# Performance work log

Measured on AMD Instinct MI355X. Metric: run time of the kernel, lower is better.

The kernel has to match this reference:

```python
import jax, jax.numpy as jnp
import numpy as np

DIM = 3456      # visual_dim
E = 1024        # embed_dim = dim_head*heads = 128*8
H = 8
D = E // H
LN_EPS = 1e-5


def _mlp(x, w1, b1, w2, b2):
    # nn.Sequential(Linear, GELU(exact), Linear)
    h = jax.nn.gelu(x @ w1.T + b1, approximate=False)
    return h @ w2.T + b2


def _ln(x, g, b):
    m = jnp.mean(x, axis=-1, keepdims=True)
    v = jnp.mean((x - m) ** 2, axis=-1, keepdims=True)
    return (x - m) * jax.lax.rsqrt(v + LN_EPS) * g + b


def setup_inputs() -> dict:
    key = jax.random.key(0)
    ks = jax.random.split(key, 24)
    std = 0.02
    d = {"x": jax.random.normal(ks[0], (5, 729, DIM), dtype=jnp.float32)}
    i = 1
    for name in ("q", "k", "v"):
        d[f"{name}_w1"] = std * jax.random.normal(ks[i], (E, DIM), dtype=jnp.float32); i += 1
        d[f"{name}_b1"] = jnp.zeros((E,), jnp.float32)
        d[f"{name}_w2"] = std * jax.random.normal(ks[i], (E, E), dtype=jnp.float32); i += 1
        d[f"{name}_b2"] = jnp.zeros((E,), jnp.float32)
        d[f"ln_{name}_g"] = jnp.ones((E,), jnp.float32)
        d[f"ln_{name}_b"] = jnp.zeros((E,), jnp.float32)
    d["in_proj_w"] = std * jax.random.normal(ks[i], (3 * E, E), dtype=jnp.float32); i += 1
    d["in_proj_b"] = jnp.zeros((3 * E,), jnp.float32)
    d["out_proj_w"] = std * jax.random.normal(ks[i], (E, E), dtype=jnp.float32); i += 1
    d["out_proj_b"] = jnp.zeros((E,), jnp.float32)
    d["to_out_w"] = std * jax.random.normal(ks[i], (DIM, E), dtype=jnp.float32)
    return d


def reference(x,
              q_w1, q_b1, q_w2, q_b2, ln_q_g, ln_q_b,
              k_w1, k_b1, k_w2, k_b2, ln_k_g, ln_k_b,
              v_w1, v_b1, v_w2, v_b2, ln_v_g, ln_v_b,
              in_proj_w, in_proj_b, out_proj_w, out_proj_b, to_out_w):
    t, hw, c = x.shape
    # spatial_temporal pattern: x_multi = x, no interpolation.
    # q/k/v: MLP -> LN -> permute(1,0,2) -> divide_feature -> flatten.
    # divide_feature is a pure permutation of tokens; all tokens end up in a
    # single (L, 1, E) attention, so full attention over the flattened
    # (hw, t) token order computes the identical result.
    q = _ln(_mlp(x, q_w1, q_b1, q_w2, q_b2), ln_q_g, ln_q_b)  # (t, hw, E)
    k = _ln(_mlp(x, k_w1, k_b1, k_w2, k_b2), ln_k_g, ln_k_b)
    v = _ln(_mlp(x, v_w1, v_b1, v_w2, v_b2), ln_v_g, ln_v_b)
    L = t * hw
    q = q.transpose(1, 0, 2).reshape(L, E)  # (hw*t, E), (h,w,t)-major order
    k = k.transpose(1, 0, 2).reshape(L, E)
    v = v.transpose(1, 0, 2).reshape(L, E)
    # nn.MultiheadAttention with packed in_proj
    qp = (q @ in_proj_w[:E].T + in_proj_b[:E]).reshape(L, H, D)
    kp = (k @ in_proj_w[E:2 * E].T + in_proj_b[E:2 * E]).reshape(L, H, D)
    vp = (v @ in_proj_w[2 * E:].T + in_proj_b[2 * E:]).reshape(L, H, D)
    scale = 1.0 / jnp.sqrt(jnp.asarray(D, q.dtype))
    scores = jnp.einsum('qhd,khd->hqk', qp, kp) * scale  # (H, L, L)
    attn = jax.nn.softmax(scores, axis=-1)
    o = jnp.einsum('hqk,khd->qhd', attn, vp).reshape(L, E)
    o = o @ out_proj_w.T + out_proj_b
    o = o.reshape(hw, t, E).transpose(1, 0, 2)  # (t, hw, E)
    out = o @ to_out_w.T                         # (t, hw, c)
    return x + out
```

## Files before the change

kernel.cpp:

```cpp
#include <hip/hip_runtime.h>
#include <hip/hip_bf16.h>

#define L_TOK 3645
#define MP    3712
#define DIMV  3456
#define EDIM  1024

typedef __attribute__((ext_vector_type(8))) short bf8;
typedef __attribute__((ext_vector_type(4))) short s4v;
typedef __attribute__((ext_vector_type(4))) float f4;

__device__ __forceinline__ short f2b(float f) {
  union { float f; unsigned u; } v; v.f = f;
  unsigned r = v.u + 0x7fffu + ((v.u >> 16) & 1u);
  return (short)(r >> 16);
}
__device__ __forceinline__ float b2f(short s) {
  union { unsigned u; float f; } v; v.u = ((unsigned)(unsigned short)s) << 16;
  return v.f;
}
__device__ __forceinline__ void gld16(const void* g, void* l) {
  __builtin_amdgcn_global_load_lds(
      (const __attribute__((address_space(1))) void*)(unsigned long long)g,
      (__attribute__((address_space(3))) void*)(unsigned)(unsigned long long)l,
      16, 0, 0);
}

__global__ __launch_bounds__(256) void k_cvt(const float* __restrict__ src,
                                             short* __restrict__ dst, int n4) {
  int i = blockIdx.x * 256 + threadIdx.x;
  if (i >= n4) return;
  float4 v = ((const float4*)src)[i];
  s4v o; o[0] = f2b(v.x); o[1] = f2b(v.y); o[2] = f2b(v.z); o[3] = f2b(v.w);
  ((s4v*)dst)[i] = o;
}
__global__ __launch_bounds__(256) void k_cvt_pad(const float* __restrict__ src,
                                                 short* __restrict__ dst, int n4src, int n4tot) {
  int i = blockIdx.x * 256 + threadIdx.x;
  if (i >= n4tot) return;
  s4v o; o[0] = 0; o[1] = 0; o[2] = 0; o[3] = 0;
  if (i < n4src) {
    float4 v = ((const float4*)src)[i];
    o[0] = f2b(v.x); o[1] = f2b(v.y); o[2] = f2b(v.z); o[3] = f2b(v.w);
  }
  ((s4v*)dst)[i] = o;
}

#define GM_GELU   0
#define GM_BIAS   1
#define GM_QSCALE 2
#define GM_RESID  3

template<int MODE>
__global__ __launch_bounds__(512, 2)
void k_gemm2(const short* __restrict__ A, long sA,
             const short* __restrict__ B, long sB,
             const float* __restrict__ bias0, const float* __restrict__ bias1,
             const float* __restrict__ bias2,
             void* __restrict__ Cout, long sC,
             int N, int K, const float* __restrict__ resid)
{
  __shared__ short L[2][2][2][8192];
  const int tid = threadIdx.x;
  const int z = blockIdx.z;
  const int brow = blockIdx.y * 256;
  const int bcol = blockIdx.x * 256;
  const short* Ab = A + (long)z * sA;
  const short* Bb = B + (long)z * sB;
  const float* bias = (z == 0) ? bias0 : (z == 1 ? bias1 : bias2);

  const int wave = tid >> 6, lane = tid & 63;
  const int lg = lane >> 4, lc = lane & 15;
  const int wm = wave >> 2, wn = wave & 3;

  const int r0 = tid >> 3, x0 = tid & 7;
  const int c1 = tid + 512;
  const int r1 = c1 >> 3, x1 = c1 & 7;
  const short* pa[2][2];
  const short* pb[2][2];
#pragma unroll
  for (int half = 0; half < 2; ++half) {
    int ra0 = brow + half * 128 + r0; if (ra0 > MP - 1) ra0 = MP - 1;
    int ra1 = brow + half * 128 + r1; if (ra1 > MP - 1) ra1 = MP - 1;
    int rb0 = bcol + half * 128 + r0; if (rb0 > N - 1) rb0 = N - 1;
    int rb1 = bcol + half * 128 + r1; if (rb1 > N - 1) rb1 = N - 1;
    pa[half][0] = Ab + (long)ra0 * K + ((x0 ^ (r0 & 7)) * 8);
    pa[half][1] = Ab + (long)ra1 * K + ((x1 ^ (r1 & 7)) * 8);
    pb[half][0] = Bb + (long)rb0 * K + ((x0 ^ (r0 & 7)) * 8);
    pb[half][1] = Bb + (long)rb1 * K + ((x1 ^ (r1 & 7)) * 8);
  }

  f4 acc[8][4];
  f4 zero = {0.f, 0.f, 0.f, 0.f};
#pragma unroll
  for (int i = 0; i < 8; ++i)
#pragma unroll
    for (int j = 0; j < 4; ++j) acc[i][j] = zero;

  auto STG = [&](int bufi, int ab, int half) {
    if (ab == 0) {
      gld16(pa[half][0], &L[bufi][0][half][tid * 8]);
      gld16(pa[half][1], &L[bufi][0][half][c1 * 8]);
      pa[half][0] += 64; pa[half][1] += 64;
    } else {
      gld16(pb[half][0], &L[bufi][1][half][tid * 8]);
      gld16(pb[half][1], &L[bufi][1][half][c1 * 8]);
      pb[half][0] += 64; pb[half][1] += 64;
    }
  };

  const int NT = K >> 6;
  STG(0, 0, 0); STG(0, 0, 1); STG(0, 1, 0); STG(0, 1, 1);

  const int bhalf = wn >> 1, brw = (wn & 1) * 64;
  bf8 bfr[4][2];

  for (int kt = 0; kt < NT; ++kt) {
    const int buf = kt & 1, nb = buf ^ 1;
    const bool more = (kt + 1 < NT);
#pragma unroll
    for (int p = 0; p < 4; ++p) {
      if (p == 0) {
        if (more) { STG(nb, 0, 0); asm volatile("s_waitcnt vmcnt(2)" ::: "memory"); }
        else      { asm volatile("s_waitcnt vmcnt(0)" ::: "memory"); }
        __builtin_amdgcn_sched_barrier(0);
        __builtin_amdgcn_s_barrier();
        __builtin_amdgcn_sched_barrier(0);
#pragma unroll
        for (int nf = 0; nf < 4; ++nf)
#pragma unroll
          for (int ks = 0; ks < 2; ++ks) {
            int row = brw + nf * 16 + lc;
            int seg = (ks * 4 + lg) ^ (row & 7);
            bfr[nf][ks] = *(const bf8*)&L[buf][1][bhalf][row * 64 + seg * 8];
          }
      } else {
        if (more) STG(nb, p >> 1, p & 1);
      }
      bf8 af[2][2];
#pragma unroll
      for (int m2 = 0; m2 < 2; ++m2)
#pragma unroll
        for (int ks = 0; ks < 2; ++ks) {
          int row = p * 32 + m2 * 16 + lc;
          int seg = (ks * 4 + lg) ^ (row & 7);
          af[m2][ks] = *(const bf8*)&L[buf][0][wm][row * 64 + seg * 8];
        }
      asm volatile("s_waitcnt lgkmcnt(0)" ::: "memory");
      __builtin_amdgcn_sched_barrier(0);
      __builtin_amdgcn_s_setprio(1);
#pragma unroll
      for (int m2 = 0; m2 < 2; ++m2)
#pragma unroll
        for (int nf = 0; nf < 4; ++nf)
#pragma unroll
          for (int ks = 0; ks < 2; ++ks)
            acc[p * 2 + m2][nf] = __builtin_amdgcn_mfma_f32_16x16x32_bf16(
                af[m2][ks], bfr[nf][ks], acc[p * 2 + m2][nf], 0, 0, 0);
      __builtin_amdgcn_s_setprio(0);
      __builtin_amdgcn_sched_barrier(0);
      __builtin_amdgcn_s_barrier();
    }
  }

  if (MODE == GM_RESID) {
    float* C = (float*)Cout;
#pragma unroll
    for (int nf = 0; nf < 4; ++nf) {
      int col = bcol + wn * 64 + nf * 16 + lc;
#pragma unroll
      for (int mf = 0; mf < 8; ++mf)
#pragma unroll
        for (int r = 0; r < 4; ++r) {
          int row = brow + wm * 128 + mf * 16 + lg * 4 + r;
          if (row < L_TOK && col < N)
            C[(long)row * N + col] = acc[mf][nf][r] + resid[(long)row * N + col];
        }
    }
  } else {
    short* C = (short*)Cout + (long)z * sC;
    const float alpha = (MODE == GM_QSCALE && z == 0) ? 0.08838834764831845f : 1.0f;
#pragma unroll
    for (int nf = 0; nf < 4; ++nf) {
      int col = bcol + wn * 64 + nf * 16 + lc;
      float bv = bias[col];
#pragma unroll
      for (int mf = 0; mf < 8; ++mf)
#pragma unroll
        for (int r = 0; r < 4; ++r) {
          int row = brow + wm * 128 + mf * 16 + lg * 4 + r;
          float v = acc[mf][nf][r] + bv;
          if (MODE == GM_GELU) v = 0.5f * v * (1.f + erff(v * 0.70710678118654752f));
          v *= alpha;
          if (row < MP) C[(long)row * EDIM + col] = f2b(v);
        }
    }
  }
}

template<int MODE>
__global__ __launch_bounds__(256)
void k_gemm(const short* __restrict__ A, long sA,
            const short* __restrict__ B, long sB,
            const float* __restrict__ bias0, const float* __restrict__ bias1,
            const float* __restrict__ bias2,
            void* __restrict__ Cout, long sC,
            int N, int K, const float* __restrict__ resid)
{
  __shared__ short As[2][128 * 32];
  __shared__ short Bs[2][128 * 32];
  const int tid  = threadIdx.x;
  const int z    = blockIdx.z;
  const int nwg  = gridDim.x * gridDim.y;
  const int orig = blockIdx.y * gridDim.x + blockIdx.x;
  const int qq   = nwg >> 3, rr = nwg & 7;
  const int xcd  = orig & 7, ofs = orig >> 3;
  const int swz  = (xcd < rr ? xcd * (qq + 1) : rr * (qq + 1) + (xcd - rr) * qq) + ofs;
  const int brow = (swz / gridDim.x) * 128;
  const int bcol = (swz % gridDim.x) * 128;

  const short* Ab = A + (long)z * sA;
  const short* Bb = B + (long)z * sB;
  const float* bias = (z == 0) ? bias0 : (z == 1 ? bias1 : bias2);

  const int wave = tid >> 6, lane = tid & 63;
  const int lg = lane >> 4, lc = lane & 15;
  const int m0 = (wave >> 1) * 64, n0 = (wave & 1) * 64;

  const int r0 = tid >> 2, seg = tid & 3;
  const int r1 = r0 + 64;
  const int so0 = (seg ^ ((r0 >> 1) & 3)) * 8;
  const int so1 = (seg ^ ((r1 >> 1) & 3)) * 8;
  const short* pA0 = Ab + (long)(brow + r0) * K + so0;
  const short* pA1 = Ab + (long)(brow + r1) * K + so1;
  const short* pB0 = Bb + (long)(bcol + r0) * K + so0;
  const short* pB1 = Bb + (long)(bcol + r1) * K + so1;

  f4 acc[4][4];
  f4 zero = {0.f, 0.f, 0.f, 0.f};
#pragma unroll
  for (int i = 0; i < 4; ++i)
#pragma unroll
    for (int j = 0; j < 4; ++j) acc[i][j] = zero;

  auto STAGE = [&](int buf) {
    gld16(pA0, &As[buf][tid * 8]);
    gld16(pA1, &As[buf][(tid + 256) * 8]);
    gld16(pB0, &Bs[buf][tid * 8]);
    gld16(pB1, &Bs[buf][(tid + 256) * 8]);
    pA0 += 32; pA1 += 32; pB0 += 32; pB1 += 32;
  };

  const int NT = K >> 5;
  STAGE(0);
  for (int t = 0; t < NT; ++t) {
    const int buf = t & 1;
    asm volatile("s_waitcnt vmcnt(0)" ::: "memory");
    __builtin_amdgcn_sched_barrier(0);
    __builtin_amdgcn_s_barrier();
    if (t + 1 < NT) STAGE((t + 1) & 1);
    const short* Al = &As[buf][0];
    const short* Bl = &Bs[buf][0];
    bf8 af[4], bfr[4];
#pragma unroll
    for (int mi = 0; mi < 4; ++mi) {
      int r = m0 + mi * 16 + lc;
      af[mi] = *(const bf8*)&Al[r * 32 + ((lg ^ ((r >> 1) & 3)) * 8)];
    }
#pragma unroll
    for (int ni = 0; ni < 4; ++ni) {
      int r = n0 + ni * 16 + lc;
      bfr[ni] = *(const bf8*)&Bl[r * 32 + ((lg ^ ((r >> 1) & 3)) * 8)];
    }
    __builtin_amdgcn_s_setprio(1);
#pragma unroll
    for (int mi = 0; mi < 4; ++mi)
#pragma unroll
      for (int ni = 0; ni < 4; ++ni)
        acc[mi][ni] = __builtin_amdgcn_mfma_f32_16x16x32_bf16(af[mi], bfr[ni], acc[mi][ni], 0, 0, 0);
    __builtin_amdgcn_s_setprio(0);
    __builtin_amdgcn_sched_barrier(0);
  }

  if (MODE == GM_RESID) {
    float* C = (float*)Cout;
#pragma unroll
    for (int ni = 0; ni < 4; ++ni) {
      int col = bcol + n0 + ni * 16 + lc;
#pragma unroll
      for (int mi = 0; mi < 4; ++mi)
#pragma unroll
        for (int r = 0; r < 4; ++r) {
          int row = brow + m0 + mi * 16 + lg * 4 + r;
          if (row < L_TOK)
            C[(long)row * N + col] = acc[mi][ni][r] + resid[(long)row * N + col];
        }
    }
  } else {
    short* C = (short*)Cout + (long)z * sC;
    const float alpha = (MODE == GM_QSCALE && z == 0) ? 0.08838834764831845f : 1.0f;
#pragma unroll
    for (int ni = 0; ni < 4; ++ni) {
      int col = bcol + n0 + ni * 16 + lc;
      float bv = bias[col];
#pragma unroll
      for (int mi = 0; mi < 4; ++mi)
#pragma unroll
        for (int r = 0; r < 4; ++r) {
          int row = brow + m0 + mi * 16 + lg * 4 + r;
          float v = acc[mi][ni][r] + bv;
          if (MODE == GM_GELU) v = 0.5f * v * (1.f + erff(v * 0.70710678118654752f));
          v *= alpha;
          C[(long)row * EDIM + col] = f2b(v);
        }
    }
  }
}

__global__ __launch_bounds__(256)
void k_ln(const short* __restrict__ A, short* __restrict__ Y,
          const float* __restrict__ g0, const float* __restrict__ g1, const float* __restrict__ g2,
          const float* __restrict__ b0, const float* __restrict__ b1, const float* __restrict__ b2)
{
  const int row = blockIdx.x, z = blockIdx.y;
  const float* g = (z == 0) ? g0 : (z == 1 ? g1 : g2);
  const float* b = (z == 0) ? b0 : (z == 1 ? b1 : b2);
  const short* a = A + ((long)z * MP + row) * EDIM;
  short* y = Y + ((long)z * MP + row) * EDIM;
  const int t = threadIdx.x;
  s4v v = *(const s4v*)&a[t * 4];
  float x0 = b2f(v[0]), x1 = b2f(v[1]), x2 = b2f(v[2]), x3 = b2f(v[3]);
  float s = x0 + x1 + x2 + x3;
  float q = x0 * x0 + x1 * x1 + x2 * x2 + x3 * x3;
#pragma unroll
  for (int off = 1; off < 64; off <<= 1) { s += __shfl_xor(s, off); q += __shfl_xor(q, off); }
  __shared__ float rs[4], rq[4];
  if ((t & 63) == 0) { rs[t >> 6] = s; rq[t >> 6] = q; }
  __syncthreads();
  s = rs[0] + rs[1] + rs[2] + rs[3];
  q = rq[0] + rq[1] + rq[2] + rq[3];
  float mean = s * (1.f / 1024.f);
  float var  = q * (1.f / 1024.f) - mean * mean;
  float rstd = rsqrtf(var + 1e-5f);
  s4v o;
#pragma unroll
  for (int j = 0; j < 4; ++j) {
    int col = t * 4 + j;
    o[j] = f2b((b2f(v[j]) - mean) * rstd * g[col] + b[col]);
  }
  *(s4v*)&y[t * 4] = o;
}

__global__ __launch_bounds__(256)
void k_vtrans(const short* __restrict__ vp, short* __restrict__ vpT)
{
  const int kb = blockIdx.x * 64, h = blockIdx.y;
  __shared__ short T[64 * 128];
  const int tid = threadIdx.x;
#pragma unroll
  for (int i = 0; i < 4; ++i) {
    int c = tid + 256 * i;
    int r = c >> 4, x = c & 15;
    bf8 val = *(const bf8*)&vp[(long)(kb + r) * EDIM + h * 128 + x * 8];
    *(bf8*)&T[r * 128 + ((x ^ (r & 7)) * 8)] = val;
  }
  __syncthreads();
#pragma unroll
  for (int i = 0; i < 4; ++i) {
    int c = tid + 256 * i;
    int dr = c >> 3, x = c & 7;
    short tmp[8];
#pragma unroll
    for (int e = 0; e < 8; ++e) {
      int kv = x * 8 + e;
      tmp[e] = T[kv * 128 + (((dr >> 3) ^ (kv & 7)) << 3) + (dr & 7)];
    }
    *(bf8*)&vpT[((long)h * 128 + dr) * MP + kb + x * 8] = *(bf8*)tmp;
  }
}

__global__ __launch_bounds__(256)
void k_attn(const short* __restrict__ qp, const short* __restrict__ kp,
            const short* __restrict__ vpT,
            short* __restrict__ op0, short* __restrict__ op1,
            float* __restrict__ lsums)
{
  const int bx = blockIdx.x;
  const int h = bx & 7;
  const int t2 = bx >> 3;
  const int qi = t2 % 29, sp = t2 / 29;
  const int qb = qi * 128;
  short* opart = sp ? op1 : op0;
  const int t0 = sp ? 29 : 0, t1 = sp ? 57 : 29;

  const int tid = threadIdx.x, wave = tid >> 6, lane = tid & 63;
  const int lg = lane >> 4, lc = lane & 15;
  __shared__ short Ks[2][64 * 128];
  __shared__ short Vs[2][128 * 64];
  __shared__ short Ps[4][32 * 64];

  const int q0 = qb + wave * 32;
  bf8 qf[2][4];
#pragma unroll
  for (int g = 0; g < 2; ++g)
#pragma unroll
    for (int d4 = 0; d4 < 4; ++d4)
      qf[g][d4] = *(const bf8*)&qp[(long)(q0 + g * 16 + lc) * EDIM + h * 128 + d4 * 32 + lg * 8];

  f4 oacc[2][8];
  f4 zero = {0.f, 0.f, 0.f, 0.f};
#pragma unroll
  for (int g = 0; g < 2; ++g)
#pragma unroll
    for (int dt = 0; dt < 8; ++dt) oacc[g][dt] = zero;
  float lsum0 = 0.f, lsum1 = 0.f;

  auto STAGE = [&](short* ksb, short* vsb, int kb) {
#pragma unroll
    for (int i = 0; i < 4; ++i) {
      int c = tid + 256 * i; int r = c >> 4, x = c & 15;
      gld16(&kp[(long)(kb + r) * EDIM + h * 128 + (x ^ (r & 7)) * 8], &ksb[c * 8]);
    }
#pragma unroll
    for (int i = 0; i < 4; ++i) {
      int c = tid + 256 * i; int dr = c >> 3, x = c & 7;
      gld16(&vpT[((long)h * 128 + dr) * MP + kb + (x ^ (dr & 7)) * 8], &vsb[c * 8]);
    }
  };

  STAGE(Ks[t0 & 1], Vs[t0 & 1], t0 * 64);

  for (int t = t0; t < t1; ++t) {
    const int kb = t * 64;
    const short* ksb = Ks[t & 1];
    const short* vsb = Vs[t & 1];
    __builtin_amdgcn_s_barrier();
    if (t + 1 < t1) {
      STAGE(Ks[(t + 1) & 1], Vs[(t + 1) & 1], kb + 64);
      asm volatile("s_waitcnt vmcnt(8)" ::: "memory");
    } else {
      asm volatile("s_waitcnt vmcnt(0)" ::: "memory");
    }
    __builtin_amdgcn_sched_barrier(0);
    __builtin_amdgcn_s_barrier();
    __builtin_amdgcn_sched_barrier(0);

#pragma unroll
    for (int s = 0; s < 4; ++s) {
      const int krow = s * 16 + lc;
      bf8 kf[4];
#pragma unroll
      for (int d4 = 0; d4 < 4; ++d4)
        kf[d4] = *(const bf8*)&ksb[krow * 128 + (((d4 * 4 + lg) ^ (krow & 7)) * 8)];
      f4 sa0 = zero, sa1 = zero;
      __builtin_amdgcn_s_setprio(1);
#pragma unroll
      for (int d4 = 0; d4 < 4; ++d4) {
        sa0 = __builtin_amdgcn_mfma_f32_16x16x32_bf16(kf[d4], qf[0][d4], sa0, 0, 0, 0);
        sa1 = __builtin_amdgcn_mfma_f32_16x16x32_bf16(kf[d4], qf[1][d4], sa1, 0, 0, 0);
      }
      __builtin_amdgcn_s_setprio(0);
      const int kvb = kb + s * 16 + lg * 4;
#pragma unroll
      for (int g = 0; g < 2; ++g) {
        f4 sa = g ? sa1 : sa0;
        float p[4];
#pragma unroll
        for (int r = 0; r < 4; ++r) {
          float e = __expf(sa[r]);
          p[r] = (kvb + r < L_TOK) ? e : 0.f;
          if (g) lsum1 += p[r]; else lsum0 += p[r];
        }
        s4v pk; pk[0] = f2b(p[0]); pk[1] = f2b(p[1]); pk[2] = f2b(p[2]); pk[3] = f2b(p[3]);
        *(s4v*)&Ps[wave][(g * 16 + lc) * 64 + ((s * 16 + lg * 4) ^ ((lc & 7) << 3))] = pk;
      }
    }
    bf8 pf[2][2];
#pragma unroll
    for (int g = 0; g < 2; ++g) {
      pf[g][0] = *(const bf8*)&Ps[wave][(g * 16 + lc) * 64 + ((lg * 8) ^ ((lc & 7) << 3))];
      pf[g][1] = *(const bf8*)&Ps[wave][(g * 16 + lc) * 64 + ((32 + lg * 8) ^ ((lc & 7) << 3))];
    }
#pragma unroll
    for (int dt = 0; dt < 8; ++dt) {
      const int vrow = dt * 16 + lc;
      bf8 vf0 = *(const bf8*)&vsb[vrow * 64 + ((lg ^ (vrow & 7)) * 8)];
      bf8 vf1 = *(const bf8*)&vsb[vrow * 64 + (((4 + lg) ^ (vrow & 7)) * 8)];
      __builtin_amdgcn_s_setprio(1);
      oacc[0][dt] = __builtin_amdgcn_mfma_f32_16x16x32_bf16(pf[0][0], vf0, oacc[0][dt], 0, 0, 0);
      oacc[0][dt] = __builtin_amdgcn_mfma_f32_16x16x32_bf16(pf[0][1], vf1, oacc[0][dt], 0, 0, 0);
      oacc[1][dt] = __builtin_amdgcn_mfma_f32_16x16x32_bf16(pf[1][0], vf0, oacc[1][dt], 0, 0, 0);
      oacc[1][dt] = __builtin_amdgcn_mfma_f32_16x16x32_bf16(pf[1][1], vf1, oacc[1][dt], 0, 0, 0);
      __builtin_amdgcn_s_setprio(0);
    }
    __builtin_amdgcn_sched_barrier(0);
  }

  lsum0 += __shfl_xor(lsum0, 16);
  lsum0 += __shfl_xor(lsum0, 32);
  lsum1 += __shfl_xor(lsum1, 16);
  lsum1 += __shfl_xor(lsum1, 32);
  if (lg == 0) {
    lsums[((sp * 8) + h) * MP + q0 + lc]      = lsum0;
    lsums[((sp * 8) + h) * MP + q0 + 16 + lc] = lsum1;
  }
#pragma unroll
  for (int g = 0; g < 2; ++g)
#pragma unroll
    for (int dt = 0; dt < 8; ++dt)
#pragma unroll
      for (int r = 0; r < 4; ++r) {
        int orow = q0 + g * 16 + lg * 4 + r;
        opart[(long)orow * EDIM + h * 128 + dt * 16 + lc] = f2b(oacc[g][dt][r]);
      }
}

__global__ __launch_bounds__(256)
void k_comb(const short* __restrict__ p0, const short* __restrict__ p1,
            const float* __restrict__ ls, short* __restrict__ ob)
{
  int i = blockIdx.x * 256 + threadIdx.x;
  int q = i >> 7;
  int h = (i & 127) >> 4;
  float rinv = 1.f / (ls[h * MP + q] + ls[(8 + h) * MP + q]);
  bf8 a = ((const bf8*)p0)[i];
  bf8 b = ((const bf8*)p1)[i];
  bf8 o;
#pragma unroll
  for (int j = 0; j < 8; ++j) o[j] = f2b((b2f(a[j]) + b2f(b[j])) * rinv);
  ((bf8*)ob)[i] = o;
}

extern "C" void kernel_launch(void* const* d_in, const int* in_sizes, int n_in,
                              void* d_out, int out_size, void* d_ws, size_t ws_size,
                              hipStream_t stream)
{
  const float* x   = (const float*)d_in[0];
  const float* ipb = (const float*)d_in[20];
  const float* opb = (const float*)d_in[22];

  char* ws = (char*)d_ws;
  short* regA = (short*)(ws + 0);
  short* regB = (short*)(ws + 25657344);
  short* w1b  = (short*)(ws + 48463872);
  short* w2b  = (short*)(ws + 69697536);
  short* wpb  = (short*)(ws + 75988992);
  short* wob  = (short*)(ws + 82280448);
  short* wtb  = (short*)(ws + 84377600);
  short* vpT  = (short*)(ws + 91455488);

  short* xb  = regA;
  short* h1  = regB;
  short* aln = regA;
  short* lnq = regB;
  short* proj = regA;
  short* ob  = regB;
  short* o2  = (short*)(ws + 33259520);
  short* pt1 = o2;
  short* pt0 = (short*)(ws + 40861696);
  float* lsums = (float*)(ws + 22806528);

  k_cvt_pad<<<12528, 256, 0, stream>>>(x, xb, 3149280, 3207168);
  k_cvt<<<3456, 256, 0, stream>>>((const float*)d_in[1],  w1b,            884736);
  k_cvt<<<3456, 256, 0, stream>>>((const float*)d_in[7],  w1b + 3538944,  884736);
  k_cvt<<<3456, 256, 0, stream>>>((const float*)d_in[13], w1b + 7077888,  884736);
  k_cvt<<<1024, 256, 0, stream>>>((const float*)d_in[3],  w2b,            262144);
  k_cvt<<<1024, 256, 0, stream>>>((const float*)d_in[9],  w2b + 1048576,  262144);
  k_cvt<<<1024, 256, 0, stream>>>((const float*)d_in[15], w2b + 2097152,  262144);
  k_cvt<<<3072, 256, 0, stream>>>((const float*)d_in[19], wpb,            786432);
  k_cvt<<<1024, 256, 0, stream>>>((const float*)d_in[21], wob,            262144);
  k_cvt<<<3456, 256, 0, stream>>>((const float*)d_in[23], wtb,            884736);

  dim3 gg3(4, 15, 3);
  k_gemm2<GM_GELU><<<gg3, 512, 0, stream>>>(xb, 0, w1b, 3538944,
      (const float*)d_in[2], (const float*)d_in[8], (const float*)d_in[14],
      h1, (long)MP * EDIM, EDIM, DIMV, nullptr);
  k_gemm2<GM_BIAS><<<gg3, 512, 0, stream>>>(h1, (long)MP * EDIM, w2b, 1048576,
      (const float*)d_in[4], (const float*)d_in[10], (const float*)d_in[16],
      aln, (long)MP * EDIM, EDIM, EDIM, nullptr);
  dim3 gl(MP, 3);
  k_ln<<<gl, 256, 0, stream>>>(aln, lnq,
      (const float*)d_in[5], (const float*)d_in[11], (const float*)d_in[17],
      (const float*)d_in[6], (const float*)d_in[12], (const float*)d_in[18]);
  k_gemm2<GM_QSCALE><<<gg3, 512, 0, stream>>>(lnq, (long)MP * EDIM, wpb, 1048576,
      ipb, ipb + 1024, ipb + 2048,
      proj, (long)MP * EDIM, EDIM, EDIM, nullptr);
  dim3 gt(MP / 64, 8);
  k_vtrans<<<gt, 256, 0, stream>>>(proj + 2L * MP * EDIM, vpT);
  k_attn<<<29 * 2 * 8, 256, 0, stream>>>(proj, proj + (long)MP * EDIM, vpT,
      pt0, pt1, lsums);
  k_comb<<<(MP * EDIM / 8) / 256, 256, 0, stream>>>(pt0, pt1, lsums, ob);
  dim3 g1(8, 29, 1);
  k_gemm<GM_BIAS><<<g1, 256, 0, stream>>>(ob, 0, wob, 0,
      opb, opb, opb, o2, 0, EDIM, EDIM, nullptr);
  dim3 gg5(14, 15, 1);
  k_gemm2<GM_RESID><<<gg5, 512, 0, stream>>>(o2, 0, wtb, 0,
      nullptr, nullptr, nullptr, d_out, 0, DIMV, EDIM, x);
}
```

Before: 452.1 us.

## Replace 256x256 GEMM kernel with 128x256 tiles and XCD-aware block swizzle

Replaces the 512-thread 256x256-tile GEMM with a 256-thread 128x256-tile kernel that uses a K-step of 32, a simpler double-buffered loop and an XCD-aware workgroup remap. It is used for the first MLP layer and the final to_out projection. The second MLP layer and the in-projection fall back to the existing 128-tile k_gemm. The aim is more workgroups to fill the CUs and better L2 locality per XCD. The cost is less data reuse per tile and a coarser pipeline with a full vmcnt(0) wait every iteration.

New measurement: 526.5 us. 1.16x slower.

```diff
diff --git a/kernel.cpp b/kernel.cpp
--- a/kernel.cpp
+++ b/kernel.cpp
@@ -52,42 +52,43 @@
 #define GM_RESID  3
 
 template<int MODE>
-__global__ __launch_bounds__(512, 2)
-void k_gemm2(const short* __restrict__ A, long sA,
+__global__ __launch_bounds__(256)
+void k_gemm3(const short* __restrict__ A, long sA,
              const short* __restrict__ B, long sB,
              const float* __restrict__ bias0, const float* __restrict__ bias1,
              const float* __restrict__ bias2,
              void* __restrict__ Cout, long sC,
              int N, int K, const float* __restrict__ resid)
 {
-  __shared__ short L[2][2][2][8192];
-  const int tid = threadIdx.x;
-  const int z = blockIdx.z;
-  const int brow = blockIdx.y * 256;
-  const int bcol = blockIdx.x * 256;
+  __shared__ short As[2][128 * 32];
+  __shared__ short Bs[2][256 * 32];
+  const int tid  = threadIdx.x;
+  const int z    = blockIdx.z;
+  const int nwg  = gridDim.x * gridDim.y;
+  const int orig = blockIdx.y * gridDim.x + blockIdx.x;
+  const int qq   = nwg >> 3, rr = nwg & 7;
+  const int xcd  = orig & 7, ofs = orig >> 3;
+  const int swz  = (xcd < rr ? xcd * (qq + 1) : rr * (qq + 1) + (xcd - rr) * qq) + ofs;
+  const int brow = (swz / gridDim.x) * 128;
+  const int bcol = (swz % gridDim.x) * 256;
+
   const short* Ab = A + (long)z * sA;
   const short* Bb = B + (long)z * sB;
   const float* bias = (z == 0) ? bias0 : (z == 1 ? bias1 : bias2);
 
   const int wave = tid >> 6, lane = tid & 63;
   const int lg = lane >> 4, lc = lane & 15;
-  const int wm = wave >> 2, wn = wave & 3;
-
-  const int r0 = tid >> 3, x0 = tid & 7;
-  const int c1 = tid + 512;
-  const int r1 = c1 >> 3, x1 = c1 & 7;
-  const short* pa[2][2];
-  const short* pb[2][2];
-#pragma unroll
-  for (int half = 0; half < 2; ++half) {
-    int ra0 = brow + half * 128 + r0; if (ra0 > MP - 1) ra0 = MP - 1;
-    int ra1 = brow + half * 128 + r1; if (ra1 > MP - 1) ra1 = MP - 1;
-    int rb0 = bcol + half * 128 + r0; if (rb0 > N - 1) rb0 = N - 1;
-    int rb1 = bcol + half * 128 + r1; if (rb1 > N - 1) rb1 = N - 1;
-    pa[half][0] = Ab + (long)ra0 * K + ((x0 ^ (r0 & 7)) * 8);
-    pa[half][1] = Ab + (long)ra1 * K + ((x1 ^ (r1 & 7)) * 8);
-    pb[half][0] = Bb + (long)rb0 * K + ((x0 ^ (r0 & 7)) * 8);
-    pb[half][1] = Bb + (long)rb1 * K + ((x1 ^ (r1 & 7)) * 8);
+
+  const int rA0 = tid >> 2, seg = tid & 3;
+  const int rA1 = rA0 + 64;
+  const short* pA0 = Ab + (long)(brow + rA0) * K + ((seg ^ ((rA0 >> 1) & 3)) * 8);
+  const short* pA1 = Ab + (long)(brow + rA1) * K + ((seg ^ ((rA1 >> 1) & 3)) * 8);
+  const short* pB[4];
+#pragma unroll
+  for (int j = 0; j < 4; ++j) {
+    int rB = (tid >> 2) + j * 64;
+    int rb = bcol + rB; if (rb > N - 1) rb = N - 1;
+    pB[j] = Bb + (long)rb * K + ((seg ^ ((rB >> 1) & 3)) * 8);
   }
 
   f4 acc[8][4];
@@ -97,82 +98,56 @@
 #pragma unroll
     for (int j = 0; j < 4; ++j) acc[i][j] = zero;
 
-  auto STG = [&](int bufi, int ab, int half) {
-    if (ab == 0) {
-      gld16(pa[half][0], &L[bufi][0][half][tid * 8]);
-      gld16(pa[half][1], &L[bufi][0][half][c1 * 8]);
-      pa[half][0] += 64; pa[half][1] += 64;
-    } else {
-      gld16(pb[half][0], &L[bufi][1][half][tid * 8]);
-      gld16(pb[half][1], &L[bufi][1][half][c1 * 8]);
-      pb[half][0] += 64; pb[half][1] += 64;
+  auto STAGE = [&](int buf) {
+    gld16(pA0, &As[buf][tid * 8]);         pA0 += 32;
+    gld16(pA1, &As[buf][(tid + 256) * 8]); pA1 += 32;
+#pragma unroll
+    for (int j = 0; j < 4; ++j) {
+      gld16(pB[j], &Bs[buf][(tid + j * 256) * 8]);
+      pB[j] += 32;
     }
   };
 
-  const int NT = K >> 6;
-  STG(0, 0, 0); STG(0, 0, 1); STG(0, 1, 0); STG(0, 1, 1);
-
-  const int bhalf = wn >> 1, brw = (wn & 1) * 64;
-  bf8 bfr[4][2];
-
-  for (int kt = 0; kt < NT; ++kt) {
-    const int buf = kt & 1, nb = buf ^ 1;
-    const bool more = (kt + 1 < NT);
-#pragma unroll
-    for (int p = 0; p < 4; ++p) {
-      if (p == 0) {
-        if (more) { STG(nb, 0, 0); asm volatile("s_waitcnt vmcnt(2)" ::: "memory"); }
-        else      { asm volatile("s_waitcnt vmcnt(0)" ::: "memory"); }
-        __builtin_amdgcn_sched_barrier(0);
-        __builtin_amdgcn_s_barrier();
-        __builtin_amdgcn_sched_barrier(0);
-#pragma unroll
-        for (int nf = 0; nf < 4; ++nf)
-#pragma unroll
-          for (int ks = 0; ks < 2; ++ks) {
-            int row = brw + nf * 16 + lc;
-            int seg = (ks * 4 + lg) ^ (row & 7);
-            bfr[nf][ks] = *(const bf8*)&L[buf][1][bhalf][row * 64 + seg * 8];
-          }
-      } else {
-        if (more) STG(nb, p >> 1, p & 1);
-      }
-      bf8 af[2][2];
-#pragma unroll
-      for (int m2 = 0; m2 < 2; ++m2)
-#pragma unroll
-        for (int ks = 0; ks < 2; ++ks) {
-          int row = p * 32 + m2 * 16 + lc;
-          int seg = (ks * 4 + lg) ^ (row & 7);
-          af[m2][ks] = *(const bf8*)&L[buf][0][wm][row * 64 + seg * 8];
-        }
-      asm volatile("s_waitcnt lgkmcnt(0)" ::: "memory");
-      __builtin_amdgcn_sched_barrier(0);
-      __builtin_amdgcn_s_setprio(1);
-#pragma unroll
-      for (int m2 = 0; m2 < 2; ++m2)
-#pragma unroll
-        for (int nf = 0; nf < 4; ++nf)
-#pragma unroll
-          for (int ks = 0; ks < 2; ++ks)
-            acc[p * 2 + m2][nf] = __builtin_amdgcn_mfma_f32_16x16x32_bf16(
-                af[m2][ks], bfr[nf][ks], acc[p * 2 + m2][nf], 0, 0, 0);
-      __builtin_amdgcn_s_setprio(0);
-      __builtin_amdgcn_sched_barrier(0);
-      __builtin_amdgcn_s_barrier();
-    }
+  const int NT = K >> 5;
+  STAGE(0);
+  for (int t = 0; t < NT; ++t) {
+    const int buf = t & 1;
+    asm volatile("s_waitcnt vmcnt(0)" ::: "memory");
+    __builtin_amdgcn_sched_barrier(0);
+    __builtin_amdgcn_s_barrier();
+    if (t + 1 < NT) STAGE((t + 1) & 1);
+
+    const short* Al = &As[buf][0];
+    const short* Bl = &Bs[buf][0];
+    bf8 bfr[4];
+#pragma unroll
+    for (int nf = 0; nf < 4; ++nf) {
+      int row = wave * 64 + nf * 16 + lc;
+      bfr[nf] = *(const bf8*)&Bl[row * 32 + ((lg ^ ((row >> 1) & 3)) * 8)];
+    }
+    __builtin_amdgcn_s_setprio(1);
+#pragma unroll
+    for (int mf = 0; mf < 8; ++mf) {
+      int row = mf * 16 + lc;
+      bf8 af = *(const bf8*)&Al[row * 32 + ((lg ^ ((row >> 1) & 3)) * 8)];
+#pragma unroll
+      for (int nf = 0; nf < 4; ++nf)
+        acc[mf][nf] = __builtin_amdgcn_mfma_f32_16x16x32_bf16(af, bfr[nf], acc[mf][nf], 0, 0, 0);
+    }
+    __builtin_amdgcn_s_setprio(0);
+    __builtin_amdgcn_sched_barrier(0);
   }
 
   if (MODE == GM_RESID) {
     float* C = (float*)Cout;
 #pragma unroll
     for (int nf = 0; nf < 4; ++nf) {
-      int col = bcol + wn * 64 + nf * 16 + lc;
+      int col = bcol + wave * 64 + nf * 16 + lc;
 #pragma unroll
       for (int mf = 0; mf < 8; ++mf)
 #pragma unroll
         for (int r = 0; r < 4; ++r) {
-          int row = brow + wm * 128 + mf * 16 + lg * 4 + r;
+          int row = brow + mf * 16 + lg * 4 + r;
           if (row < L_TOK && col < N)
             C[(long)row * N + col] = acc[mf][nf][r] + resid[(long)row * N + col];
         }
@@ -182,18 +157,20 @@
     const float alpha = (MODE == GM_QSCALE && z == 0) ? 0.08838834764831845f : 1.0f;
 #pragma unroll
     for (int nf = 0; nf < 4; ++nf) {
-      int col = bcol + wn * 64 + nf * 16 + lc;
-      float bv = bias[col];
-#pragma unroll
-      for (int mf = 0; mf < 8; ++mf)
-#pragma unroll
-        for (int r = 0; r < 4; ++r) {
-          int row = brow + wm * 128 + mf * 16 + lg * 4 + r;
-          float v = acc[mf][nf][r] + bv;
-          if (MODE == GM_GELU) v = 0.5f * v * (1.f + erff(v * 0.70710678118654752f));
-          v *= alpha;
-          if (row < MP) C[(long)row * EDIM + col] = f2b(v);
-        }
+      int col = bcol + wave * 64 + nf * 16 + lc;
+      if (col < N) {
+        float bv = bias[col];
+#pragma unroll
+        for (int mf = 0; mf < 8; ++mf)
+#pragma unroll
+          for (int r = 0; r < 4; ++r) {
+            int row = brow + mf * 16 + lg * 4 + r;
+            float v = acc[mf][nf][r] + bv;
+            if (MODE == GM_GELU) v = 0.5f * v * (1.f + erff(v * 0.70710678118654752f));
+            v *= alpha;
+            C[(long)row * EDIM + col] = f2b(v);
+          }
+      }
     }
   }
 }
@@ -571,18 +548,19 @@
   k_cvt<<<1024, 256, 0, stream>>>((const float*)d_in[21], wob,            262144);
   k_cvt<<<3456, 256, 0, stream>>>((const float*)d_in[23], wtb,            884736);
 
-  dim3 gg3(4, 15, 3);
-  k_gemm2<GM_GELU><<<gg3, 512, 0, stream>>>(xb, 0, w1b, 3538944,
+  dim3 gw3(4, 29, 3);
+  k_gemm3<GM_GELU><<<gw3, 256, 0, stream>>>(xb, 0, w1b, 3538944,
       (const float*)d_in[2], (const float*)d_in[8], (const float*)d_in[14],
       h1, (long)MP * EDIM, EDIM, DIMV, nullptr);
-  k_gemm2<GM_BIAS><<<gg3, 512, 0, stream>>>(h1, (long)MP * EDIM, w2b, 1048576,
+  dim3 g3(8, 29, 3), g1(8, 29, 1);
+  k_gemm<GM_BIAS><<<g3, 256, 0, stream>>>(h1, (long)MP * EDIM, w2b, 1048576,
       (const float*)d_in[4], (const float*)d_in[10], (const float*)d_in[16],
       aln, (long)MP * EDIM, EDIM, EDIM, nullptr);
   dim3 gl(MP, 3);
   k_ln<<<gl, 256, 0, stream>>>(aln, lnq,
       (const float*)d_in[5], (const float*)d_in[11], (const float*)d_in[17],
       (const float*)d_in[6], (const float*)d_in[12], (const float*)d_in[18]);
-  k_gemm2<GM_QSCALE><<<gg3, 512, 0, stream>>>(lnq, (long)MP * EDIM, wpb, 1048576,
+  k_gemm<GM_QSCALE><<<g3, 256, 0, stream>>>(lnq, (long)MP * EDIM, wpb, 1048576,
       ipb, ipb + 1024, ipb + 2048,
       proj, (long)MP * EDIM, EDIM, EDIM, nullptr);
   dim3 gt(MP / 64, 8);
@@ -590,10 +568,9 @@
   k_attn<<<29 * 2 * 8, 256, 0, stream>>>(proj, proj + (long)MP * EDIM, vpT,
       pt0, pt1, lsums);
   k_comb<<<(MP * EDIM / 8) / 256, 256, 0, stream>>>(pt0, pt1, lsums, ob);
-  dim3 g1(8, 29, 1);
   k_gemm<GM_BIAS><<<g1, 256, 0, stream>>>(ob, 0, wob, 0,
       opb, opb, opb, o2, 0, EDIM, EDIM, nullptr);
-  dim3 gg5(14, 15, 1);
-  k_gemm2<GM_RESID><<<gg5, 512, 0, stream>>>(o2, 0, wtb, 0,
+  dim3 gw5(14, 29, 1);
+  k_gemm3<GM_RESID><<<gw5, 256, 0, stream>>>(o2, 0, wtb, 0,
       nullptr, nullptr, nullptr, d_out, 0, DIMV, EDIM, x);
 }
```
